# Optimization experiments

Measured on AMD Instinct MI355X. Metric: run time of the kernel, lower is better.

The kernel has to match this reference:

```python
import jax, jax.numpy as jnp
import numpy as np

B, N, F_IN, F_OUT = 8, 2048, 128, 64
ALPHA = 0.2  # LeakyReLU negative slope
NEG_INF = -9e15


def setup_inputs() -> dict:
    key = jax.random.key(0)
    k1, k2, k3, k4 = jax.random.split(key, 4)
    h = jax.random.normal(k1, (B, N, F_IN), dtype=jnp.float32)
    adj = jax.random.randint(k2, (B, N, N), 0, 2, dtype=jnp.int32)
    # xavier_uniform with gain=1.414 approximated by scaled normals (values are arbitrary params)
    W = jax.random.normal(k3, (F_IN, F_OUT), dtype=jnp.float32) * (1.414 * np.sqrt(2.0 / (F_IN + F_OUT)))
    a = jax.random.normal(k4, (2 * F_OUT, 1), dtype=jnp.float32) * (1.414 * np.sqrt(2.0 / (2 * F_OUT + 1)))
    return {"h": h, "adj": adj, "W": W, "a": a}


def reference(h, adj, W, a):
    # Wh: [B, N, F_out]
    Wh = jnp.einsum('bnf,fo->bno', h, W)
    Fo = W.shape[1]
    a1 = a[:Fo, 0]   # [F_out]
    a2 = a[Fo:, 0]   # [F_out]
    # e[b,i,j] = leakyrelu(Wh[b,i]@a1 + Wh[b,j]@a2)  (== cat(Wh_i,Wh_j)@a, same math, no N^2*2F blowup)
    e1 = jnp.einsum('bno,o->bn', Wh, a1)  # [B, N]
    e2 = jnp.einsum('bno,o->bn', Wh, a2)  # [B, N]
    e = e1[:, :, None] + e2[:, None, :]   # [B, N, N]
    e = jnp.where(e > 0, e, ALPHA * e)    # LeakyReLU
    e = jnp.where(adj > 0, e, NEG_INF)    # mask non-edges
    attention = jax.nn.softmax(e, axis=-1)
    # dropout is identity in inference mode (deterministic reference)
    h_prime = jnp.einsum('bij,bjo->bio', attention, Wh)  # [B, N, F_out]
    return jax.nn.elu(h_prime)  # concat=True branch
```

## Files before the change

kernel.cpp:

```cpp
#include <hip/hip_runtime.h>
#include <hip/hip_bf16.h>

#define BB 8
#define NN 2048
#define FIN 128
#define FO 64
#define ALPHA 0.2f

typedef __attribute__((ext_vector_type(8))) short bf16x8;
typedef __attribute__((ext_vector_type(4))) float f32x4;
typedef __attribute__((ext_vector_type(4))) int i32x4;

typedef __attribute__((address_space(1))) const void gvoid;
typedef __attribute__((address_space(3))) void lvoid;

__device__ inline void gl_lds16(const void* g, void* l) {
    __builtin_amdgcn_global_load_lds((gvoid*)g, (lvoid*)l, 16, 0, 0);
}

__device__ inline short f2bf(float x) {
    unsigned u = __float_as_uint(x);
    u += 0x7fffu + ((u >> 16) & 1u);
    return (short)(u >> 16);
}

__global__ __launch_bounds__(256) void wh_kernel(
    const float* __restrict__ h, const float* __restrict__ W,
    const float* __restrict__ a, float* __restrict__ e1, float* __restrict__ e2,
    short* __restrict__ whF)
{
    __shared__ float hs[32][FIN];
    const int r0 = blockIdx.x * 32;
    const int t = threadIdx.x;
    const float4* hsrc = (const float4*)(h + (size_t)r0 * FIN);
    float4* hdst = (float4*)(&hs[0][0]);
#pragma unroll
    for (int k = 0; k < 4; k++) hdst[t + 256 * k] = hsrc[t + 256 * k];
    __syncthreads();

    const int o = t & 63;
    const int wv = t >> 6;
    float acc[8];
#pragma unroll
    for (int rr = 0; rr < 8; rr++) acc[rr] = 0.f;

    for (int f = 0; f < FIN; f += 4) {
        const float w0 = W[(f + 0) * FO + o];
        const float w1 = W[(f + 1) * FO + o];
        const float w2 = W[(f + 2) * FO + o];
        const float w3 = W[(f + 3) * FO + o];
#pragma unroll
        for (int rr = 0; rr < 8; rr++) {
            float4 hv = *(const float4*)&hs[wv * 8 + rr][f];
            acc[rr] = fmaf(hv.x, w0, acc[rr]);
            acc[rr] = fmaf(hv.y, w1, acc[rr]);
            acc[rr] = fmaf(hv.z, w2, acc[rr]);
            acc[rr] = fmaf(hv.w, w3, acc[rr]);
        }
    }

    const int b   = r0 / NN;
    const int ib0 = r0 - b * NN;
    const int ibb = ib0 + wv * 8;
    const int jc  = ibb >> 5;
    const int qq  = (ibb >> 3) & 3;
    const int ot  = o >> 4, mm = o & 15;
    const int L   = mm + qq * 16;
    bf16x8 frag;
#pragma unroll
    for (int rr = 0; rr < 8; rr++) frag[rr] = f2bf(acc[rr]);
    *(bf16x8*)(whF + ((((size_t)(b * 64 + jc) * 4 + ot) * 64 + L) * 8)) = frag;

    const float a1 = a[o], a2 = a[FO + o];
#pragma unroll
    for (int rr = 0; rr < 8; rr++) {
        float v1 = acc[rr] * a1, v2 = acc[rr] * a2;
#pragma unroll
        for (int msk = 32; msk >= 1; msk >>= 1) {
            v1 += __shfl_xor(v1, msk, 64);
            v2 += __shfl_xor(v2, msk, 64);
        }
        if (o == 0) { e1[r0 + wv * 8 + rr] = v1; e2[r0 + wv * 8 + rr] = v2; }
    }
}

__global__ __launch_bounds__(256) void e2max_kernel(
    const float* __restrict__ e2, float* __restrict__ e2max)
{
    const int b = blockIdx.x;
    const int t = threadIdx.x;
    float m = -1e30f;
    for (int j = t; j < NN; j += 256) m = fmaxf(m, e2[b * NN + j]);
#pragma unroll
    for (int k = 32; k >= 1; k >>= 1) m = fmaxf(m, __shfl_xor(m, k, 64));
    __shared__ float red[4];
    if ((t & 63) == 0) red[t >> 6] = m;
    __syncthreads();
    if (t == 0) e2max[b] = fmaxf(fmaxf(red[0], red[1]), fmaxf(red[2], red[3]));
}

struct SMemS {
    int   adjs[4][4][16][8][4];
    float e2s[4][512];
};
struct SMemC { float comb[4][16][64]; float lsum[4][16]; };
union SMemU { SMemS s; SMemC c; };

struct WFrag { bf16x8 f0, f1, f2, f3; };

#define CFENCE asm volatile("" ::: "memory")
#define WAITVM_(n) asm volatile("s_waitcnt vmcnt(" #n ")" ::: "memory")
#define WAITVM(n) WAITVM_(n)

#define STAGE(k) do { \
    gl_lds16(asrc0 + (size_t)(k) * 32, &ladj[(k) & 3][0][0][0]); \
    gl_lds16(asrc1 + (size_t)(k) * 32, &ladj[(k) & 3][8][0][0]); \
    CFENCE; \
} while (0)

#define WLOAD(dst, k) do { \
    const short* bfp = whFw + (size_t)(k) * 2048; \
    dst.f0 = *(const bf16x8*)(bfp); \
    dst.f1 = *(const bf16x8*)(bfp + 512); \
    dst.f2 = *(const bf16x8*)(bfp + 1024); \
    dst.f3 = *(const bf16x8*)(bfp + 1536); \
    CFENCE; \
} while (0)

#define STEPC(k, VM, WF) do { \
    WAITVM(VM); \
    i32x4 va0 = *(const i32x4*)&ladj[(k) & 3][m][u0][0]; \
    i32x4 va1 = *(const i32x4*)&ladj[(k) & 3][m][u1][0]; \
    f32x4 ev0 = *(const f32x4*)&le2[(k) * 32 + q * 8]; \
    f32x4 ev1 = *(const f32x4*)&le2[(k) * 32 + q * 8 + 4]; \
    float pe[8]; \
    _Pragma("unroll") \
    for (int jj = 0; jj < 8; jj++) { \
        const int   av = (jj < 4) ? va0[jj] : va1[jj - 4]; \
        const float ej = (jj < 4) ? ev0[jj] : ev1[jj - 4]; \
        const float s  = fmaf(ej, L2E, E1v); \
        const float lk = fmaxf(s, ALPHA * s); \
        pe[jj] = __builtin_amdgcn_exp2f(lk + fmaf((float)av, 4000.0f, negMiB)); \
    } \
    union { unsigned u[4]; bf16x8 v; } au; \
    _Pragma("unroll") \
    for (int jj = 0; jj < 4; jj++) \
        au.u[jj] = __builtin_amdgcn_perm(__float_as_uint(pe[2 * jj + 1]), \
                                         __float_as_uint(pe[2 * jj]), 0x07060302u); \
    acc0 = __builtin_amdgcn_mfma_f32_16x16x32_bf16(au.v, WF.f0, acc0, 0, 0, 0); \
    acc1 = __builtin_amdgcn_mfma_f32_16x16x32_bf16(au.v, WF.f1, acc1, 0, 0, 0); \
    acc2 = __builtin_amdgcn_mfma_f32_16x16x32_bf16(au.v, WF.f2, acc2, 0, 0, 0); \
    acc3 = __builtin_amdgcn_mfma_f32_16x16x32_bf16(au.v, WF.f3, acc3, 0, 0, 0); \
    acc4 = __builtin_amdgcn_mfma_f32_16x16x32_bf16(au.v, ones, acc4, 0, 0, 0); \
} while (0)

__global__ __launch_bounds__(256) void attn_kernel(
    const int* __restrict__ adj, const float* __restrict__ e1,
    const float* __restrict__ e2, const float* __restrict__ e2max,
    const short* __restrict__ whF, float* __restrict__ out)
{
    __shared__ __align__(16) SMemU sm;
    const int t = threadIdx.x, w = t >> 6, lane = t & 63;
    const int m = lane & 15, q = lane >> 4;
    const int blk = blockIdx.x;
    const int b = blk >> 7, i0 = (blk & 127) * 16;

    const float L2E = 1.4426950408889634f;
    const float e1v = e1[b * NN + i0 + m];
    float mr = e1v + e2max[b];
    mr = mr > 0.f ? mr : ALPHA * mr;
    const float E1v = e1v * L2E;
    const float negMiB = -(mr * L2E + 4000.0f);

    const int l8 = lane >> 3, c7 = lane & 7;
    const int csw = (c7 ^ l8) * 4;
    const int* asrc0 = adj + ((size_t)(b * NN + i0 + l8)) * NN + w * 512 + csw;
    const int* asrc1 = asrc0 + (size_t)8 * NN;
    int (*ladj)[16][8][4] = sm.s.adjs[w];
    float* le2 = sm.s.e2s[w];
    const float* e2src = e2 + b * NN + w * 512 + lane * 4;

    const short* whFw = whF + (size_t)b * (64 * 4 * 64 * 8)
                            + (size_t)(w * 16) * 2048 + lane * 8;

    f32x4 acc0 = {0.f,0.f,0.f,0.f}, acc1 = acc0, acc2 = acc0, acc3 = acc0, acc4 = acc0;
    bf16x8 ones;
#pragma unroll
    for (int jj = 0; jj < 8; jj++) ones[jj] = (short)0x3F80;

    const int u0 = (q * 2) ^ (m & 7);
    const int u1 = u0 ^ 1;

    gl_lds16(e2src,       &le2[0]);
    gl_lds16(e2src + 256, &le2[256]);
    CFENCE;
    STAGE(0); STAGE(1); STAGE(2);
    WFrag W0f, W1f;
    WLOAD(W0f, 0); WLOAD(W1f, 1);

#pragma unroll 1
    for (int k = 0; k < 12; k += 2) {
        WFrag Wa; WLOAD(Wa, k + 2); STAGE(k + 3); STEPC(k, 18, W0f); W0f = Wa;
        WFrag Wb; WLOAD(Wb, k + 3); STAGE(k + 4); STEPC(k + 1, 18, W1f); W1f = Wb;
    }
    { WFrag Wa; WLOAD(Wa, 14); STAGE(15); STEPC(12, 18, W0f); W0f = Wa; }
    { WFrag Wb; WLOAD(Wb, 15);            STEPC(13, 16, W1f); W1f = Wb; }
    STEPC(14, 10, W0f);
    STEPC(15,  4, W1f);

    __syncthreads();
    if (m == 0) {
#pragma unroll
        for (int r = 0; r < 4; r++) sm.c.lsum[w][q * 4 + r] = acc4[r];
    }
#pragma unroll
    for (int ot = 0; ot < 4; ot++) {
        f32x4 av = (ot == 0) ? acc0 : (ot == 1) ? acc1 : (ot == 2) ? acc2 : acc3;
#pragma unroll
        for (int reg = 0; reg < 4; reg++)
            sm.c.comb[w][q * 4 + reg][ot * 16 + m] = av[reg];
    }
    __syncthreads();

    const int row = t >> 4, c0 = (t & 15) * 4;
    f32x4 sum = *(const f32x4*)&sm.c.comb[0][row][c0];
#pragma unroll
    for (int ww = 1; ww < 4; ww++) {
        f32x4 sv = *(const f32x4*)&sm.c.comb[ww][row][c0];
        sum.x += sv.x; sum.y += sv.y; sum.z += sv.z; sum.w += sv.w;
    }
    float l = sm.c.lsum[0][row] + sm.c.lsum[1][row] + sm.c.lsum[2][row] + sm.c.lsum[3][row];
    l = fmaxf(l, 1e-30f);
    const float rl = 1.f / l;
    f32x4 res;
    float vr[4] = { sum.x * rl, sum.y * rl, sum.z * rl, sum.w * rl };
#pragma unroll
    for (int kk = 0; kk < 4; kk++)
        res[kk] = vr[kk] > 0.f ? vr[kk] : (__expf(vr[kk]) - 1.f);
    *(f32x4*)&out[((size_t)(b * NN + i0 + row)) * FO + c0] = res;
}

extern "C" void kernel_launch(void* const* d_in, const int* in_sizes, int n_in,
                              void* d_out, int out_size, void* d_ws, size_t ws_size,
                              hipStream_t stream) {
    const float* h   = (const float*)d_in[0];
    const int*   adj = (const int*)d_in[1];
    const float* W   = (const float*)d_in[2];
    const float* a   = (const float*)d_in[3];
    float* out = (float*)d_out;

    char* ws = (char*)d_ws;
    short* whF = (short*)ws;
    size_t off = (size_t)BB * 64 * 4 * 64 * 8 * sizeof(short);
    float* e1  = (float*)(ws + off);  off += (size_t)BB * NN * 4;
    float* e2  = (float*)(ws + off);  off += (size_t)BB * NN * 4;
    float* e2m = (float*)(ws + off);

    wh_kernel<<<(BB * NN) / 32, 256, 0, stream>>>(h, W, a, e1, e2, whF);
    e2max_kernel<<<BB, 256, 0, stream>>>(e2, e2m);
    attn_kernel<<<BB * (NN / 16), 256, 0, stream>>>(adj, e1, e2, e2m, whF, out);
}
```

Measured before the change: 220.0 us.

## Process two 16-row tiles per block to reuse Wh fragments and e2 loads

Each attention block now covers 32 query rows instead of 16. Every wave computes two sets of scores and MFMA accumulators that share the same Wh B-fragments and e2 values, so whF and e2 traffic per row is halved. The grid shrinks to 512 blocks and the LDS adjacency buffer doubles. It also raises register pressure and adds VALU work per step, with fewer blocks available to hide latency. The adj read, which dominates the traffic, is unchanged per row.

```diff
diff --git a/kernel.cpp b/kernel.cpp
--- a/kernel.cpp
+++ b/kernel.cpp
@@ -100,10 +100,10 @@
 }
 
 struct SMemS {
-    int   adjs[4][4][16][8][4];
+    int   adjs[4][4][2][16][8][4];
     float e2s[4][512];
 };
-struct SMemC { float comb[4][16][64]; float lsum[4][16]; };
+struct SMemC { float comb[4][2][16][64]; float lsum[4][2][16]; };
 union SMemU { SMemS s; SMemC c; };
 
 struct WFrag { bf16x8 f0, f1, f2, f3; };
@@ -113,8 +113,11 @@
 #define WAITVM(n) WAITVM_(n)
 
 #define STAGE(k) do { \
-    gl_lds16(asrc0 + (size_t)(k) * 32, &ladj[(k) & 3][0][0][0]); \
-    gl_lds16(asrc1 + (size_t)(k) * 32, &ladj[(k) & 3][8][0][0]); \
+    const int bf_ = (k) & 3; \
+    gl_lds16(asrc0 + (size_t)(k) * 32, &ladj[bf_][0][0][0][0]); \
+    gl_lds16(asrc1 + (size_t)(k) * 32, &ladj[bf_][0][8][0][0]); \
+    gl_lds16(asrc2 + (size_t)(k) * 32, &ladj[bf_][1][0][0][0]); \
+    gl_lds16(asrc3 + (size_t)(k) * 32, &ladj[bf_][1][8][0][0]); \
     CFENCE; \
 } while (0)
 
@@ -127,31 +130,44 @@
     CFENCE; \
 } while (0)
 
-#define STEPC(k, VM, WF) do { \
-    WAITVM(VM); \
-    i32x4 va0 = *(const i32x4*)&ladj[(k) & 3][m][u0][0]; \
-    i32x4 va1 = *(const i32x4*)&ladj[(k) & 3][m][u1][0]; \
-    f32x4 ev0 = *(const f32x4*)&le2[(k) * 32 + q * 8]; \
-    f32x4 ev1 = *(const f32x4*)&le2[(k) * 32 + q * 8 + 4]; \
+#define SCORE8(AU, VA0, VA1, E1C, NMB) do { \
     float pe[8]; \
     _Pragma("unroll") \
     for (int jj = 0; jj < 8; jj++) { \
-        const int   av = (jj < 4) ? va0[jj] : va1[jj - 4]; \
+        const int   av = (jj < 4) ? VA0[jj] : VA1[jj - 4]; \
         const float ej = (jj < 4) ? ev0[jj] : ev1[jj - 4]; \
-        const float s  = fmaf(ej, L2E, E1v); \
+        const float s  = fmaf(ej, L2E, E1C); \
         const float lk = fmaxf(s, ALPHA * s); \
-        pe[jj] = __builtin_amdgcn_exp2f(lk + fmaf((float)av, 4000.0f, negMiB)); \
+        pe[jj] = __builtin_amdgcn_exp2f(lk + fmaf((float)av, 4000.0f, NMB)); \
     } \
-    union { unsigned u[4]; bf16x8 v; } au; \
     _Pragma("unroll") \
     for (int jj = 0; jj < 4; jj++) \
-        au.u[jj] = __builtin_amdgcn_perm(__float_as_uint(pe[2 * jj + 1]), \
+        AU.u[jj] = __builtin_amdgcn_perm(__float_as_uint(pe[2 * jj + 1]), \
                                          __float_as_uint(pe[2 * jj]), 0x07060302u); \
-    acc0 = __builtin_amdgcn_mfma_f32_16x16x32_bf16(au.v, WF.f0, acc0, 0, 0, 0); \
-    acc1 = __builtin_amdgcn_mfma_f32_16x16x32_bf16(au.v, WF.f1, acc1, 0, 0, 0); \
-    acc2 = __builtin_amdgcn_mfma_f32_16x16x32_bf16(au.v, WF.f2, acc2, 0, 0, 0); \
-    acc3 = __builtin_amdgcn_mfma_f32_16x16x32_bf16(au.v, WF.f3, acc3, 0, 0, 0); \
-    acc4 = __builtin_amdgcn_mfma_f32_16x16x32_bf16(au.v, ones, acc4, 0, 0, 0); \
+} while (0)
+
+#define STEPC(k, VM, WF) do { \
+    WAITVM(VM); \
+    const int bf_ = (k) & 3; \
+    i32x4 va00 = *(const i32x4*)&ladj[bf_][0][m][u0][0]; \
+    i32x4 va01 = *(const i32x4*)&ladj[bf_][0][m][u1][0]; \
+    i32x4 va10 = *(const i32x4*)&ladj[bf_][1][m][u0][0]; \
+    i32x4 va11 = *(const i32x4*)&ladj[bf_][1][m][u1][0]; \
+    f32x4 ev0 = *(const f32x4*)&le2[(k) * 32 + q * 8]; \
+    f32x4 ev1 = *(const f32x4*)&le2[(k) * 32 + q * 8 + 4]; \
+    union { unsigned u[4]; bf16x8 v; } au0, au1; \
+    SCORE8(au0, va00, va01, E1v0, negMiB0); \
+    SCORE8(au1, va10, va11, E1v1, negMiB1); \
+    acc00 = __builtin_amdgcn_mfma_f32_16x16x32_bf16(au0.v, WF.f0, acc00, 0, 0, 0); \
+    acc01 = __builtin_amdgcn_mfma_f32_16x16x32_bf16(au0.v, WF.f1, acc01, 0, 0, 0); \
+    acc02 = __builtin_amdgcn_mfma_f32_16x16x32_bf16(au0.v, WF.f2, acc02, 0, 0, 0); \
+    acc03 = __builtin_amdgcn_mfma_f32_16x16x32_bf16(au0.v, WF.f3, acc03, 0, 0, 0); \
+    acc04 = __builtin_amdgcn_mfma_f32_16x16x32_bf16(au0.v, ones, acc04, 0, 0, 0); \
+    acc10 = __builtin_amdgcn_mfma_f32_16x16x32_bf16(au1.v, WF.f0, acc10, 0, 0, 0); \
+    acc11 = __builtin_amdgcn_mfma_f32_16x16x32_bf16(au1.v, WF.f1, acc11, 0, 0, 0); \
+    acc12 = __builtin_amdgcn_mfma_f32_16x16x32_bf16(au1.v, WF.f2, acc12, 0, 0, 0); \
+    acc13 = __builtin_amdgcn_mfma_f32_16x16x32_bf16(au1.v, WF.f3, acc13, 0, 0, 0); \
+    acc14 = __builtin_amdgcn_mfma_f32_16x16x32_bf16(au1.v, ones, acc14, 0, 0, 0); \
 } while (0)
 
 __global__ __launch_bounds__(256) void attn_kernel(
@@ -163,27 +179,34 @@
     const int t = threadIdx.x, w = t >> 6, lane = t & 63;
     const int m = lane & 15, q = lane >> 4;
     const int blk = blockIdx.x;
-    const int b = blk >> 7, i0 = (blk & 127) * 16;
+    const int b = blk >> 6, i0 = (blk & 63) * 32;
 
     const float L2E = 1.4426950408889634f;
-    const float e1v = e1[b * NN + i0 + m];
-    float mr = e1v + e2max[b];
-    mr = mr > 0.f ? mr : ALPHA * mr;
-    const float E1v = e1v * L2E;
-    const float negMiB = -(mr * L2E + 4000.0f);
+    const float e2m = e2max[b];
+    const float e1v0 = e1[b * NN + i0 + m];
+    const float e1v1 = e1[b * NN + i0 + 16 + m];
+    float mr0 = e1v0 + e2m; mr0 = mr0 > 0.f ? mr0 : ALPHA * mr0;
+    float mr1 = e1v1 + e2m; mr1 = mr1 > 0.f ? mr1 : ALPHA * mr1;
+    const float E1v0 = e1v0 * L2E, E1v1 = e1v1 * L2E;
+    const float negMiB0 = -(mr0 * L2E + 4000.0f);
+    const float negMiB1 = -(mr1 * L2E + 4000.0f);
 
     const int l8 = lane >> 3, c7 = lane & 7;
     const int csw = (c7 ^ l8) * 4;
     const int* asrc0 = adj + ((size_t)(b * NN + i0 + l8)) * NN + w * 512 + csw;
     const int* asrc1 = asrc0 + (size_t)8 * NN;
-    int (*ladj)[16][8][4] = sm.s.adjs[w];
+    const int* asrc2 = asrc0 + (size_t)16 * NN;
+    const int* asrc3 = asrc0 + (size_t)24 * NN;
+    int (*ladj)[2][16][8][4] = sm.s.adjs[w];
     float* le2 = sm.s.e2s[w];
     const float* e2src = e2 + b * NN + w * 512 + lane * 4;
 
     const short* whFw = whF + (size_t)b * (64 * 4 * 64 * 8)
                             + (size_t)(w * 16) * 2048 + lane * 8;
 
-    f32x4 acc0 = {0.f,0.f,0.f,0.f}, acc1 = acc0, acc2 = acc0, acc3 = acc0, acc4 = acc0;
+    f32x4 z = {0.f,0.f,0.f,0.f};
+    f32x4 acc00 = z, acc01 = z, acc02 = z, acc03 = z, acc04 = z;
+    f32x4 acc10 = z, acc11 = z, acc12 = z, acc13 = z, acc14 = z;
     bf16x8 ones;
 #pragma unroll
     for (int jj = 0; jj < 8; jj++) ones[jj] = (short)0x3F80;
@@ -200,44 +223,57 @@
 
 #pragma unroll 1
     for (int k = 0; k < 12; k += 2) {
-        WFrag Wa; WLOAD(Wa, k + 2); STAGE(k + 3); STEPC(k, 18, W0f); W0f = Wa;
-        WFrag Wb; WLOAD(Wb, k + 3); STAGE(k + 4); STEPC(k + 1, 18, W1f); W1f = Wb;
-    }
-    { WFrag Wa; WLOAD(Wa, 14); STAGE(15); STEPC(12, 18, W0f); W0f = Wa; }
-    { WFrag Wb; WLOAD(Wb, 15);            STEPC(13, 16, W1f); W1f = Wb; }
-    STEPC(14, 10, W0f);
+        WFrag Wa; WLOAD(Wa, k + 2); STAGE(k + 3); STEPC(k, 20, W0f); W0f = Wa;
+        WFrag Wb; WLOAD(Wb, k + 3); STAGE(k + 4); STEPC(k + 1, 20, W1f); W1f = Wb;
+    }
+    { WFrag Wa; WLOAD(Wa, 14); STAGE(15); STEPC(12, 20, W0f); W0f = Wa; }
+    { WFrag Wb; WLOAD(Wb, 15);            STEPC(13, 20, W1f); W1f = Wb; }
+    STEPC(14, 12, W0f);
     STEPC(15,  4, W1f);
 
     __syncthreads();
     if (m == 0) {
 #pragma unroll
-        for (int r = 0; r < 4; r++) sm.c.lsum[w][q * 4 + r] = acc4[r];
+        for (int r = 0; r < 4; r++) {
+            sm.c.lsum[w][0][q * 4 + r] = acc04[r];
+            sm.c.lsum[w][1][q * 4 + r] = acc14[r];
+        }
     }
 #pragma unroll
     for (int ot = 0; ot < 4; ot++) {
-        f32x4 av = (ot == 0) ? acc0 : (ot == 1) ? acc1 : (ot == 2) ? acc2 : acc3;
-#pragma unroll
-        for (int reg = 0; reg < 4; reg++)
-            sm.c.comb[w][q * 4 + reg][ot * 16 + m] = av[reg];
-    }
-    __syncthreads();
-
-    const int row = t >> 4, c0 = (t & 15) * 4;
-    f32x4 sum = *(const f32x4*)&sm.c.comb[0][row][c0];
-#pragma unroll
-    for (int ww = 1; ww < 4; ww++) {
-        f32x4 sv = *(const f32x4*)&sm.c.comb[ww][row][c0];
-        sum.x += sv.x; sum.y += sv.y; sum.z += sv.z; sum.w += sv.w;
-    }
-    float l = sm.c.lsum[0][row] + sm.c.lsum[1][row] + sm.c.lsum[2][row] + sm.c.lsum[3][row];
-    l = fmaxf(l, 1e-30f);
-    const float rl = 1.f / l;
-    f32x4 res;
-    float vr[4] = { sum.x * rl, sum.y * rl, sum.z * rl, sum.w * rl };
-#pragma unroll
-    for (int kk = 0; kk < 4; kk++)
-        res[kk] = vr[kk] > 0.f ? vr[kk] : (__expf(vr[kk]) - 1.f);
-    *(f32x4*)&out[((size_t)(b * NN + i0 + row)) * FO + c0] = res;
+        f32x4 a0 = (ot == 0) ? acc00 : (ot == 1) ? acc01 : (ot == 2) ? acc02 : acc03;
+        f32x4 a1 = (ot == 0) ? acc10 : (ot == 1) ? acc11 : (ot == 2) ? acc12 : acc13;
+#pragma unroll
+        for (int reg = 0; reg < 4; reg++) {
+            sm.c.comb[w][0][q * 4 + reg][ot * 16 + m] = a0[reg];
+            sm.c.comb[w][1][q * 4 + reg][ot * 16 + m] = a1[reg];
+        }
+    }
+    __syncthreads();
+
+#pragma unroll
+    for (int it = 0; it < 2; it++) {
+        const int idx = t + it * 256;
+        const int row = idx >> 4;
+        const int tl = row >> 4, r16 = row & 15;
+        const int c0 = (idx & 15) * 4;
+        f32x4 sum = *(const f32x4*)&sm.c.comb[0][tl][r16][c0];
+#pragma unroll
+        for (int ww = 1; ww < 4; ww++) {
+            f32x4 sv = *(const f32x4*)&sm.c.comb[ww][tl][r16][c0];
+            sum.x += sv.x; sum.y += sv.y; sum.z += sv.z; sum.w += sv.w;
+        }
+        float l = sm.c.lsum[0][tl][r16] + sm.c.lsum[1][tl][r16]
+                + sm.c.lsum[2][tl][r16] + sm.c.lsum[3][tl][r16];
+        l = fmaxf(l, 1e-30f);
+        const float rl = 1.f / l;
+        f32x4 res;
+        float vr[4] = { sum.x * rl, sum.y * rl, sum.z * rl, sum.w * rl };
+#pragma unroll
+        for (int kk = 0; kk < 4; kk++)
+            res[kk] = vr[kk] > 0.f ? vr[kk] : (__expf(vr[kk]) - 1.f);
+        *(f32x4*)&out[((size_t)(b * NN + i0 + row)) * FO + c0] = res;
+    }
 }
 
 extern "C" void kernel_launch(void* const* d_in, const int* in_sizes, int n_in,
@@ -258,5 +294,5 @@
 
     wh_kernel<<<(BB * NN) / 32, 256, 0, stream>>>(h, W, a, e1, e2, whF);
     e2max_kernel<<<BB, 256, 0, stream>>>(e2, e2m);
-    attn_kernel<<<BB * (NN / 16), 256, 0, stream>>>(adj, e1, e2, e2m, whF, out);
-}
+    attn_kernel<<<BB * (NN / 32), 256, 0, stream>>>(adj, e1, e2, e2m, whF, out);
+}
```

Result: no change. 219.3 us (-0.3%).
